# Kernel optimization log

Hardware: AMD Instinct MI355X
Metric: run time of the kernel (lower is better)

## Reference

```python
import jax, jax.numpy as jnp
import numpy as np

V_FEATS = 1024; N1 = 800; N2 = 800; K = 10
CONV = [256, 128]; DENSE = [256, 64]


def setup_inputs() -> dict:
    key = jax.random.key(0)
    ks = jax.random.split(key, 20)
    inp = {
        "Z1": jax.random.normal(ks[0], (N1, V_FEATS), jnp.float32),
        "nb1": jax.random.randint(ks[2], (N1, K), -1, N1),
        "Z2": jax.random.normal(ks[1], (N2, V_FEATS), jnp.float32),
        "nb2": jax.random.randint(ks[3], (N2, K), -1, N2),
    }
    j = 4
    dims = [V_FEATS] + CONV
    for i, (di, do) in enumerate(zip(dims[:-1], dims[1:])):
        s = 1.0 / np.sqrt(di)
        inp[f"Wr{i}"] = jax.random.normal(ks[j], (di, do), jnp.float32) * s; j += 1
        inp[f"Wnr{i}"] = jax.random.normal(ks[j], (di, do), jnp.float32) * s; j += 1
    fdims = [2 * CONV[-1]] + DENSE + [1]
    for i, (di, do) in enumerate(zip(fdims[:-1], fdims[1:])):
        s = 1.0 / np.sqrt(di)
        inp[f"fW{i}"] = jax.random.normal(ks[j], (di, do), jnp.float32) * s; j += 1
        inp[f"fb{i}"] = jnp.zeros((do,), jnp.float32)
    return inp


def gnn_layer(Z, nb, Wr, Wnr):
    # residue (self) signal and neighbor base signal
    res = Z @ Wr                                  # [N, F]
    base = Z @ Wnr                                # [N, F]
    mask = nb > -1                                # [N, K]
    feats = base[nb] * mask[..., None]            # gather (neg idx wrap, masked out)
    norm = jnp.maximum(mask.sum(1), 1).astype(Z.dtype)  # [N], avoid div-by-0
    return jax.nn.relu(res + feats.sum(1) / norm[:, None])


def _forward(Z1, nb1, Z2, nb2, Wr0, Wnr0, Wr1, Wnr1, fW0, fb0, fW1, fb1, fW2, fb2):
    # two stacked GNN layers per protein (shared weights across the two proteins)
    x1 = gnn_layer(gnn_layer(Z1, nb1, Wr0, Wnr0), nb1, Wr1, Wnr1)  # [N1, F]
    x2 = gnn_layer(gnn_layer(Z2, nb2, Wr0, Wnr0), nb2, Wr1, Wnr1)  # [N2, F]
    n1, F = x1.shape
    n2 = x2.shape[0]
    # all-pairs concat: itertools.product(rows(x1), rows(x2)) -> [N1*N2, 2F]
    pairs = jnp.concatenate(
        [jnp.broadcast_to(x1[:, None, :], (n1, n2, F)),
         jnp.broadcast_to(x2[None, :, :], (n1, n2, F))], axis=-1
    ).reshape(n1 * n2, 2 * F)
    h = jax.nn.relu(pairs @ fW0 + fb0)
    h = jax.nn.relu(h @ fW1 + fb1)
    return jnp.squeeze(h @ fW2 + fb2)             # [N1*N2]


def reference(Z1, nb1, Z2, nb2, Wr0, Wnr0, Wr1, Wnr1, fW0, fb0, fW1, fb1, fW2, fb2):
    return _forward(Z1, nb1, Z2, nb2, Wr0, Wnr0, Wr1, Wnr1,
                    fW0, fb0, fW1, fb1, fW2, fb2)
```

## Files before the change

### kernel.cpp

```cpp
#include <hip/hip_runtime.h>
#include <hip/hip_bf16.h>
#include <cstdint>
#include <cstddef>


typedef __bf16 bf16_t;
typedef __bf16 bf16x4 __attribute__((ext_vector_type(4)));
typedef __bf16 bf16x8 __attribute__((ext_vector_type(8)));
typedef float f32x4 __attribute__((ext_vector_type(4)));
typedef _Float16 f16_t;
typedef _Float16 f16x8 __attribute__((ext_vector_type(8)));

static __device__ __forceinline__ f32x4 mfma_bf16(bf16x8 a, bf16x8 b, f32x4 c) {
  return __builtin_amdgcn_mfma_f32_16x16x32_bf16(a, b, c, 0, 0, 0);
}
static __device__ __forceinline__ f32x4 mfma_f16(f16x8 a, f16x8 b, f32x4 c) {
  return __builtin_amdgcn_mfma_f32_16x16x32_f16(a, b, c, 0, 0, 0);
}

#define N1R 800
#define NR  1600
#define VF  1024
#define F0  256
#define F1  128

static __device__ __forceinline__ void split8(float4 va, float4 vb,
                                              bf16x8& h8, bf16x8& l8) {
  float v[8] = {va.x, va.y, va.z, va.w, vb.x, vb.y, vb.z, vb.w};
  #pragma unroll
  for (int e = 0; e < 8; ++e) {
    bf16_t h = (bf16_t)v[e];
    h8[e] = h;
    l8[e] = (bf16_t)(v[e] - (float)h);
  }
}

__global__ void conv_agg(const float* __restrict__ Z1, const float* __restrict__ Z2,
                         const int* __restrict__ nb1, const int* __restrict__ nb2,
                         const float* __restrict__ Wr0, const float* __restrict__ Wnr0,
                         const float* __restrict__ Wr1, const float* __restrict__ Wnr1,
                         const float* __restrict__ fW0, const float* __restrict__ fW1,
                         const float* __restrict__ fb1, const float* __restrict__ fW2,
                         const float* __restrict__ fb2,
                         bf16_t* __restrict__ W0h, bf16_t* __restrict__ W0l,
                         bf16_t* __restrict__ W1h, bf16_t* __restrict__ W1l,
                         bf16_t* __restrict__ fAh, bf16_t* __restrict__ fAl,
                         bf16_t* __restrict__ fBh, bf16_t* __restrict__ fBl,
                         f16_t* __restrict__ fW1th, float* __restrict__ fbw,
                         bf16_t* __restrict__ Zah, bf16_t* __restrict__ Zal) {
  int wb = blockIdx.x;
  int tid = threadIdx.x;
  if (wb >= 2625) {
    int r = wb - 2625;
    const int* nbp;
    const float* Zp;
    if (r < N1R) { nbp = nb1 + r * 10; Zp = Z1; }
    else         { nbp = nb2 + (r - N1R) * 10; Zp = Z2; }
    int c4 = tid * 4;
    float4 s = make_float4(0.f, 0.f, 0.f, 0.f);
    int cnt = 0;
    #pragma unroll
    for (int k = 0; k < 10; ++k) {
      int idx = nbp[k];
      if (idx > -1) {
        cnt++;
        float4 v = *(const float4*)(Zp + (size_t)idx * VF + c4);
        s.x += v.x; s.y += v.y; s.z += v.z; s.w += v.w;
      }
    }
    float inv = 1.f / (float)(cnt > 0 ? cnt : 1);
    float vv[4] = {s.x * inv, s.y * inv, s.z * inv, s.w * inv};
    bf16x4 h4, l4;
    #pragma unroll
    for (int e = 0; e < 4; ++e) {
      bf16_t h = (bf16_t)vv[e];
      h4[e] = h;
      l4[e] = (bf16_t)(vv[e] - (float)h);
    }
    *(bf16x4*)(Zah + (size_t)r * VF + c4) = h4;
    *(bf16x4*)(Zal + (size_t)r * VF + c4) = l4;
    return;
  }
  if (wb >= 2560 && wb < 2624) {
    int t = (wb - 2560) * 256 + tid;
    int n = t & 63;
    int k = t >> 6;
    fW1th[(n << 8) + k] = (f16_t)fW1[k * 64 + n];
    return;
  }
  if (wb == 2624) {
    if (tid < 128) {
      int jl = tid & 15, s = tid >> 4;
      fbw[jl * 8 + s] = (s < 4) ? fb1[s * 16 + jl] : fW2[(s - 4) * 16 + jl];
    } else if (tid == 128) {
      fbw[128] = fb2[0];
    }
    return;
  }
  const float* src; bf16_t* dh; bf16_t* dl; int ld, lk, ln, b0;
  if      (wb < 1024) { src = Wr0;  ld = 256; lk = 10; ln = 8; dh = W0h;              dl = W0l;              b0 = 0;    }
  else if (wb < 2048) { src = Wnr0; ld = 256; lk = 10; ln = 8; dh = W0h + 256 * 1024; dl = W0l + 256 * 1024; b0 = 1024; }
  else if (wb < 2176) { src = Wr1;  ld = 128; lk = 8;  ln = 7; dh = W1h;              dl = W1l;              b0 = 2048; }
  else if (wb < 2304) { src = Wnr1; ld = 128; lk = 8;  ln = 7; dh = W1h + 128 * 256;  dl = W1l + 128 * 256;  b0 = 2176; }
  else if (wb < 2432) { src = fW0;             ld = 256; lk = 7; ln = 8; dh = fAh;    dl = fAl;              b0 = 2304; }
  else                { src = fW0 + 128 * 256; ld = 256; lk = 7; ln = 8; dh = fBh;    dl = fBl;              b0 = 2432; }
  int t = (wb - b0) * 256 + tid;
  int n = t & ((1 << ln) - 1);
  int k = t >> ln;
  float v = src[k * ld + n];
  bf16_t h = (bf16_t)v;
  dh[(n << lk) + k] = h;
  dl[(n << lk) + k] = (bf16_t)(v - (float)h);
}

#define STEP6(ah, al, b0h, b0l, b1h, b1l)        \
  acc0 = mfma_bf16(ah, b0h, acc0);               \
  acc1 = mfma_bf16(ah, b1h, acc1);               \
  acc0 = mfma_bf16(al, b0h, acc0);               \
  acc1 = mfma_bf16(al, b1h, acc1);               \
  acc0 = mfma_bf16(ah, b0l, acc0);               \
  acc1 = mfma_bf16(ah, b1l, acc1);

__global__ __launch_bounds__(256) void gemm_l1(
    const float* __restrict__ Z1, const float* __restrict__ Z2,
    const bf16_t* __restrict__ Zah, const bf16_t* __restrict__ Zal,
    const bf16_t* __restrict__ W0h, const bf16_t* __restrict__ W0l,
    bf16_t* __restrict__ H0h, bf16_t* __restrict__ H0l) {
  int lane = threadIdx.x & 63;
  int w = threadIdx.x >> 6;
  int wr = w >> 1, wc = w & 1;
  int jl = lane & 15, hi = lane >> 4;

  int row0 = blockIdx.y * 32 + wr * 16;
  int col0 = blockIdx.x * 64 + wc * 32;
  int r = row0 + jl;
  int c0 = col0 + jl, c1 = col0 + 16 + jl;

  const float* pZ = ((r < N1R) ? Z1 + (size_t)r * VF
                               : Z2 + (size_t)(r - N1R) * VF) + hi * 8;
  const bf16_t* pAh = Zah + (size_t)r * VF + hi * 8;
  const bf16_t* pAl = Zal + (size_t)r * VF + hi * 8;
  const bf16_t* pB0h = W0h + (size_t)c0 * 1024 + hi * 8;
  const bf16_t* pB1h = W0h + (size_t)c1 * 1024 + hi * 8;
  const bf16_t* pB0l = W0l + (size_t)c0 * 1024 + hi * 8;
  const bf16_t* pB1l = W0l + (size_t)c1 * 1024 + hi * 8;
  const size_t OFF = (size_t)256 * 1024;

  f32x4 acc0 = {}, acc1 = {};
  for (int kb = 0; kb < 1024; kb += 32) {
    bf16x8 ah, al;
    split8(*(const float4*)(pZ + kb), *(const float4*)(pZ + kb + 4), ah, al);
    bf16x8 b0h = *(const bf16x8*)(pB0h + kb);
    bf16x8 b1h = *(const bf16x8*)(pB1h + kb);
    bf16x8 b0l = *(const bf16x8*)(pB0l + kb);
    bf16x8 b1l = *(const bf16x8*)(pB1l + kb);
    STEP6(ah, al, b0h, b0l, b1h, b1l)
  }
  for (int kb = 0; kb < 1024; kb += 32) {
    bf16x8 ah = *(const bf16x8*)(pAh + kb);
    bf16x8 al = *(const bf16x8*)(pAl + kb);
    bf16x8 b0h = *(const bf16x8*)(pB0h + OFF + kb);
    bf16x8 b1h = *(const bf16x8*)(pB1h + OFF + kb);
    bf16x8 b0l = *(const bf16x8*)(pB0l + OFF + kb);
    bf16x8 b1l = *(const bf16x8*)(pB1l + OFF + kb);
    STEP6(ah, al, b0h, b0l, b1h, b1l)
  }

  f32x4 accs[2] = {acc0, acc1};
  #pragma unroll
  for (int nn = 0; nn < 2; ++nn) {
    int col = col0 + nn * 16 + jl;
    #pragma unroll
    for (int reg = 0; reg < 4; ++reg) {
      int row = row0 + hi * 4 + reg;
      float v = fmaxf(accs[nn][reg], 0.f);
      bf16_t h = (bf16_t)v;
      H0h[(size_t)row * F0 + col] = h;
      H0l[(size_t)row * F0 + col] = (bf16_t)(v - (float)h);
    }
  }
}

__global__ void agg1_kernel(const bf16_t* __restrict__ H0h, const bf16_t* __restrict__ H0l,
                            const int* __restrict__ nb1, const int* __restrict__ nb2,
                            bf16_t* __restrict__ Gah, bf16_t* __restrict__ Gal) {
  int r = blockIdx.x;
  int c = threadIdx.x;
  const int* nbp;
  int roff;
  if (r < N1R) { nbp = nb1 + r * 10; roff = 0; }
  else         { nbp = nb2 + (r - N1R) * 10; roff = N1R; }
  float s = 0.f; int cnt = 0;
  #pragma unroll
  for (int k = 0; k < 10; ++k) {
    int idx = nbp[k];
    if (idx > -1) {
      cnt++;
      size_t o = (size_t)(roff + idx) * F0 + c;
      s += (float)H0h[o] + (float)H0l[o];
    }
  }
  float v = s / (float)(cnt > 0 ? cnt : 1);
  bf16_t h = (bf16_t)v;
  Gah[(size_t)r * F0 + c] = h;
  Gal[(size_t)r * F0 + c] = (bf16_t)(v - (float)h);
}

__global__ __launch_bounds__(256) void gemm_l2(
    const bf16_t* __restrict__ H0h, const bf16_t* __restrict__ H0l,
    const bf16_t* __restrict__ Gah, const bf16_t* __restrict__ Gal,
    const bf16_t* __restrict__ W1h, const bf16_t* __restrict__ W1l,
    bf16_t* __restrict__ H1h, bf16_t* __restrict__ H1l) {
  int lane = threadIdx.x & 63;
  int w = threadIdx.x >> 6;
  int wr = w >> 1, wc = w & 1;
  int jl = lane & 15, hi = lane >> 4;

  int row0 = blockIdx.y * 32 + wr * 16;
  int col0 = blockIdx.x * 64 + wc * 32;
  int r = row0 + jl;
  int c0 = col0 + jl, c1 = col0 + 16 + jl;

  const bf16_t* pAh = H0h + (size_t)r * F0 + hi * 8;
  const bf16_t* pAl = H0l + (size_t)r * F0 + hi * 8;
  const bf16_t* pGh = Gah + (size_t)r * F0 + hi * 8;
  const bf16_t* pGl = Gal + (size_t)r * F0 + hi * 8;
  const bf16_t* pB0h = W1h + (size_t)c0 * 256 + hi * 8;
  const bf16_t* pB1h = W1h + (size_t)c1 * 256 + hi * 8;
  const bf16_t* pB0l = W1l + (size_t)c0 * 256 + hi * 8;
  const bf16_t* pB1l = W1l + (size_t)c1 * 256 + hi * 8;
  const size_t OFF = (size_t)128 * 256;

  f32x4 acc0 = {}, acc1 = {};
  for (int kb = 0; kb < 256; kb += 32) {
    bf16x8 ah = *(const bf16x8*)(pAh + kb);
    bf16x8 al = *(const bf16x8*)(pAl + kb);
    bf16x8 b0h = *(const bf16x8*)(pB0h + kb);
    bf16x8 b1h = *(const bf16x8*)(pB1h + kb);
    bf16x8 b0l = *(const bf16x8*)(pB0l + kb);
    bf16x8 b1l = *(const bf16x8*)(pB1l + kb);
    STEP6(ah, al, b0h, b0l, b1h, b1l)
  }
  for (int kb = 0; kb < 256; kb += 32) {
    bf16x8 ah = *(const bf16x8*)(pGh + kb);
    bf16x8 al = *(const bf16x8*)(pGl + kb);
    bf16x8 b0h = *(const bf16x8*)(pB0h + OFF + kb);
    bf16x8 b1h = *(const bf16x8*)(pB1h + OFF + kb);
    bf16x8 b0l = *(const bf16x8*)(pB0l + OFF + kb);
    bf16x8 b1l = *(const bf16x8*)(pB1l + OFF + kb);
    STEP6(ah, al, b0h, b0l, b1h, b1l)
  }

  f32x4 accs[2] = {acc0, acc1};
  #pragma unroll
  for (int nn = 0; nn < 2; ++nn) {
    int col = col0 + nn * 16 + jl;
    #pragma unroll
    for (int reg = 0; reg < 4; ++reg) {
      int row = row0 + hi * 4 + reg;
      float v = fmaxf(accs[nn][reg], 0.f);
      bf16_t h = (bf16_t)v;
      H1h[(size_t)row * F1 + col] = h;
      H1l[(size_t)row * F1 + col] = (bf16_t)(v - (float)h);
    }
  }
}

static __device__ __forceinline__ void gemm_body(
    const bf16_t* __restrict__ Ah, const bf16_t* __restrict__ Al,
    const bf16_t* __restrict__ Bth, const bf16_t* __restrict__ Btl,
    const float* __restrict__ bias, f16_t* __restrict__ Ch,
    int M, int N, int K, int row0b, int col0b) {
  int lane = threadIdx.x & 63;
  int w = threadIdx.x >> 6;
  int wr = w >> 1, wc = w & 1;
  int jl = lane & 15, hi = lane >> 4;

  int row0 = row0b + wr * 32;
  int col0 = col0b + wc * 32;

  int r0 = min(row0 + jl, M - 1);
  int r1 = min(row0 + 16 + jl, M - 1);
  int c0 = col0 + jl;
  int c1 = col0 + 16 + jl;

  const bf16_t* pA0h = Ah + (size_t)r0 * K + hi * 8;
  const bf16_t* pA1h = Ah + (size_t)r1 * K + hi * 8;
  const bf16_t* pA0l = Al + (size_t)r0 * K + hi * 8;
  const bf16_t* pA1l = Al + (size_t)r1 * K + hi * 8;
  const bf16_t* pB0h = Bth + (size_t)c0 * K + hi * 8;
  const bf16_t* pB1h = Bth + (size_t)c1 * K + hi * 8;
  const bf16_t* pB0l = Btl + (size_t)c0 * K + hi * 8;
  const bf16_t* pB1l = Btl + (size_t)c1 * K + hi * 8;

  f32x4 acc[2][2] = {};
  for (int kb = 0; kb < K; kb += 32) {
    bf16x8 a0h = *(const bf16x8*)(pA0h + kb);
    bf16x8 a1h = *(const bf16x8*)(pA1h + kb);
    bf16x8 a0l = *(const bf16x8*)(pA0l + kb);
    bf16x8 a1l = *(const bf16x8*)(pA1l + kb);
    bf16x8 b0h = *(const bf16x8*)(pB0h + kb);
    bf16x8 b1h = *(const bf16x8*)(pB1h + kb);
    bf16x8 b0l = *(const bf16x8*)(pB0l + kb);
    bf16x8 b1l = *(const bf16x8*)(pB1l + kb);

    acc[0][0] = mfma_bf16(a0h, b0h, acc[0][0]);
    acc[0][1] = mfma_bf16(a0h, b1h, acc[0][1]);
    acc[1][0] = mfma_bf16(a1h, b0h, acc[1][0]);
    acc[1][1] = mfma_bf16(a1h, b1h, acc[1][1]);

    acc[0][0] = mfma_bf16(a0l, b0h, acc[0][0]);
    acc[0][1] = mfma_bf16(a0l, b1h, acc[0][1]);
    acc[1][0] = mfma_bf16(a1l, b0h, acc[1][0]);
    acc[1][1] = mfma_bf16(a1l, b1h, acc[1][1]);

    acc[0][0] = mfma_bf16(a0h, b0l, acc[0][0]);
    acc[0][1] = mfma_bf16(a0h, b1l, acc[0][1]);
    acc[1][0] = mfma_bf16(a1h, b0l, acc[1][0]);
    acc[1][1] = mfma_bf16(a1h, b1l, acc[1][1]);
  }

  #pragma unroll
  for (int m = 0; m < 2; ++m) {
    #pragma unroll
    for (int nn = 0; nn < 2; ++nn) {
      int col = col0 + nn * 16 + jl;
      float bv = bias ? bias[col] : 0.f;
      #pragma unroll
      for (int reg = 0; reg < 4; ++reg) {
        int row = row0 + m * 16 + hi * 4 + reg;
        if (row < M) Ch[(size_t)row * N + col] = (f16_t)(acc[m][nn][reg] + bv);
      }
    }
  }
}

__global__ __launch_bounds__(256) void gemm_dual(
    const bf16_t* __restrict__ H1h, const bf16_t* __restrict__ H1l,
    const bf16_t* __restrict__ fAh, const bf16_t* __restrict__ fAl,
    const bf16_t* __restrict__ fBh, const bf16_t* __restrict__ fBl,
    const float* __restrict__ fb0, f16_t* __restrict__ ABh) {
  int part = blockIdx.y / 13;
  int my = blockIdx.y % 13;
  gemm_body(H1h + (size_t)part * N1R * F1, H1l + (size_t)part * N1R * F1,
            part ? fBh : fAh, part ? fBl : fAl, part ? nullptr : fb0,
            ABh + (size_t)part * N1R * 256, N1R, 256, F1,
            my * 64, blockIdx.x * 64);
}

#define IBLK 2
#define ITILE 16
__global__ __launch_bounds__(256) void pair_kernel(
    const f16_t* __restrict__ ABh, const f16_t* __restrict__ W1th,
    const float* __restrict__ fbw, float* __restrict__ out) {
  __shared__ alignas(16) unsigned char sWh[64 * 512];
  __shared__ alignas(16) f16_t sA[ITILE * 256];

  const int tid = threadIdx.x;
  const int lane = tid & 63;
  const int w = tid >> 6;
  const int jl = lane & 15;
  const int hi = lane >> 4;
  const int j0 = blockIdx.x * 64;
  const int i0 = blockIdx.y * ITILE;

  #pragma unroll
  for (int s = 0; s < 8; ++s) {
    int c = tid + 256 * s;
    int n = c >> 5;
    int cb = (c & 31) << 4;
    int sw = cb ^ ((n & 7) << 4);
    *(uint4*)(sWh + n * 512 + sw) = *(const uint4*)((const unsigned char*)W1th + n * 512 + cb);
  }
  #pragma unroll
  for (int s = 0; s < 2; ++s) {
    int c = tid + 256 * s;
    int rr = c >> 5;
    int cc = c & 31;
    *(uint4*)((unsigned char*)sA + rr * 512 + cc * 16) =
        *(const uint4*)(ABh + (size_t)(i0 + rr) * 256 + cc * 8);
  }

  int j = j0 + w * 16 + jl;
  f16x8 breg[8];
  {
    const f16_t* Bp = ABh + (size_t)(N1R + j) * 256;
    bool ok = (j < N1R);
    f16x8 z{};
    #pragma unroll
    for (int t = 0; t < 8; ++t)
      breg[t] = ok ? *(const f16x8*)(Bp + t * 32 + hi * 8) : z;
  }

  float4 fb1r = *(const float4*)(fbw + jl * 8);
  float4 fw2r = *(const float4*)(fbw + jl * 8 + 4);
  float bias2 = fbw[128];

  __syncthreads();

  #pragma unroll 1
  for (int ig = 0; ig < ITILE / IBLK; ++ig) {
    f32x4 acc[IBLK][4] = {};
    #pragma unroll
    for (int t = 0; t < 8; ++t) {
      f16x8 bv = breg[t];
      f16x8 af[IBLK];
      const f16x8 Zv{};
      #pragma unroll
      for (int ib = 0; ib < IBLK; ++ib) {
        f16x8 av = *(const f16x8*)(sA + (ig * IBLK + ib) * 256 + t * 32 + hi * 8);
        af[ib] = __builtin_elementwise_max(av + bv, Zv);
      }
      int kbyte = t * 64 + hi * 16;
      #pragma unroll
      for (int nf = 0; nf < 4; ++nf) {
        int n = nf * 16 + jl;
        f16x8 wh = *(const f16x8*)(sWh + n * 512 + (kbyte ^ ((n & 7) << 4)));
        #pragma unroll
        for (int ib = 0; ib < IBLK; ++ib)
          acc[ib][nf] = mfma_f16(af[ib], wh, acc[ib][nf]);
      }
    }
    float fb1a[4] = {fb1r.x, fb1r.y, fb1r.z, fb1r.w};
    float fw2a[4] = {fw2r.x, fw2r.y, fw2r.z, fw2r.w};
    #pragma unroll
    for (int ib = 0; ib < IBLK; ++ib) {
      float part[4];
      #pragma unroll
      for (int r = 0; r < 4; ++r) {
        float ssum = 0.f;
        #pragma unroll
        for (int nf = 0; nf < 4; ++nf) {
          float h = acc[ib][nf][r] + fb1a[nf];
          h = fmaxf(h, 0.f);
          ssum += h * fw2a[nf];
        }
        part[r] = ssum;
      }
      #pragma unroll
      for (int off = 1; off < 16; off <<= 1) {
        #pragma unroll
        for (int r = 0; r < 4; ++r) part[r] += __shfl_xor(part[r], off, 64);
      }
      if (jl == 0) {
        int jo = j0 + w * 16 + hi * 4;
        if (jo < N1R) {
          float4 o = make_float4(part[0] + bias2, part[1] + bias2,
                                 part[2] + bias2, part[3] + bias2);
          *(float4*)(out + (size_t)(i0 + ig * IBLK + ib) * 800 + jo) = o;
        }
      }
    }
  }
}

extern "C" void kernel_launch(void* const* d_in, const int* in_sizes, int n_in,
                              void* d_out, int out_size, void* d_ws, size_t ws_size,
                              hipStream_t stream) {
  const float* Z1   = (const float*)d_in[0];
  const int*   nb1  = (const int*)d_in[1];
  const float* Z2   = (const float*)d_in[2];
  const int*   nb2  = (const int*)d_in[3];
  const float* Wr0  = (const float*)d_in[4];
  const float* Wnr0 = (const float*)d_in[5];
  const float* Wr1  = (const float*)d_in[6];
  const float* Wnr1 = (const float*)d_in[7];
  const float* fW0  = (const float*)d_in[8];
  const float* fb0  = (const float*)d_in[9];
  const float* fW1  = (const float*)d_in[10];
  const float* fb1  = (const float*)d_in[11];
  const float* fW2  = (const float*)d_in[12];
  const float* fb2  = (const float*)d_in[13];
  float* out = (float*)d_out;

  char* p = (char*)d_ws;
  auto alloc = [&](size_t bytes) {
    char* q = p;
    p += (bytes + 255) & ~(size_t)255;
    return q;
  };
  bf16_t* W0h   = (bf16_t*)alloc((size_t)512 * 1024 * 2);
  bf16_t* W0l   = (bf16_t*)alloc((size_t)512 * 1024 * 2);
  bf16_t* W1h   = (bf16_t*)alloc((size_t)256 * 256 * 2);
  bf16_t* W1l   = (bf16_t*)alloc((size_t)256 * 256 * 2);
  bf16_t* fAh   = (bf16_t*)alloc((size_t)256 * 128 * 2);
  bf16_t* fAl   = (bf16_t*)alloc((size_t)256 * 128 * 2);
  bf16_t* fBh   = (bf16_t*)alloc((size_t)256 * 128 * 2);
  bf16_t* fBl   = (bf16_t*)alloc((size_t)256 * 128 * 2);
  f16_t*  fW1th = (f16_t*)alloc((size_t)64 * 256 * 2);
  float*  fbw   = (float*)alloc(129 * 4);
  bf16_t* Zah   = (bf16_t*)alloc((size_t)NR * VF * 2);
  bf16_t* Zal   = (bf16_t*)alloc((size_t)NR * VF * 2);
  bf16_t* H0h   = (bf16_t*)alloc((size_t)NR * F0 * 2);
  bf16_t* H0l   = (bf16_t*)alloc((size_t)NR * F0 * 2);
  bf16_t* Gah   = (bf16_t*)alloc((size_t)NR * F0 * 2);
  bf16_t* Gal   = (bf16_t*)alloc((size_t)NR * F0 * 2);
  bf16_t* H1h   = (bf16_t*)alloc((size_t)NR * F1 * 2);
  bf16_t* H1l   = (bf16_t*)alloc((size_t)NR * F1 * 2);
  f16_t*  ABh   = (f16_t*)alloc((size_t)NR * 256 * 2);
  (void)in_sizes; (void)n_in; (void)out_size; (void)ws_size;

  conv_agg<<<4225, 256, 0, stream>>>(Z1, Z2, nb1, nb2, Wr0, Wnr0, Wr1, Wnr1,
                                     fW0, fW1, fb1, fW2, fb2,
                                     W0h, W0l, W1h, W1l, fAh, fAl, fBh, fBl,
                                     fW1th, fbw, Zah, Zal);
  gemm_l1<<<dim3(4, 50), 256, 0, stream>>>(Z1, Z2, Zah, Zal, W0h, W0l, H0h, H0l);
  agg1_kernel<<<NR, 256, 0, stream>>>(H0h, H0l, nb1, nb2, Gah, Gal);
  gemm_l2<<<dim3(2, 50), 256, 0, stream>>>(H0h, H0l, Gah, Gal, W1h, W1l, H1h, H1l);
  gemm_dual<<<dim3(4, 26), 256, 0, stream>>>(H1h, H1l, fAh, fAl, fBh, fBl, fb0, ABh);
  pair_kernel<<<dim3(13, 50), 256, 0, stream>>>(ABh, fW1th, fbw, out);
}
```

Before: 120.4 us.

## Split layer-1 GEMM over K into fp32 partials and shrink GEMM tiles

The first-layer GEMM is split along its two K halves, the raw Z part and the aggregated Z part, using a third grid dimension. Each half writes fp32 partial sums, and the aggregation kernel now adds them, applies ReLU and makes the bf16 hi/lo split. The l1, l2 and dual GEMMs all move to 16x64 tiles with one 16x16 MFMA tile per wave, which multiplies the block count. This is meant to fill the 256 CUs, which the old 100–200 block grids left idle. In exchange it adds fp32 partial-buffer traffic, makes the neighbor gather read two fp32 arrays, and gives up operand reuse per wave.

```diff
diff --git a/kernel.cpp b/kernel.cpp
--- a/kernel.cpp
+++ b/kernel.cpp
@@ -113,83 +113,76 @@
   dl[(n << lk) + k] = (bf16_t)(v - (float)h);
 }
 
-#define STEP6(ah, al, b0h, b0l, b1h, b1l)        \
-  acc0 = mfma_bf16(ah, b0h, acc0);               \
-  acc1 = mfma_bf16(ah, b1h, acc1);               \
-  acc0 = mfma_bf16(al, b0h, acc0);               \
-  acc1 = mfma_bf16(al, b1h, acc1);               \
-  acc0 = mfma_bf16(ah, b0l, acc0);               \
-  acc1 = mfma_bf16(ah, b1l, acc1);
-
 __global__ __launch_bounds__(256) void gemm_l1(
     const float* __restrict__ Z1, const float* __restrict__ Z2,
     const bf16_t* __restrict__ Zah, const bf16_t* __restrict__ Zal,
     const bf16_t* __restrict__ W0h, const bf16_t* __restrict__ W0l,
-    bf16_t* __restrict__ H0h, bf16_t* __restrict__ H0l) {
+    float* __restrict__ P) {
   int lane = threadIdx.x & 63;
   int w = threadIdx.x >> 6;
-  int wr = w >> 1, wc = w & 1;
   int jl = lane & 15, hi = lane >> 4;
 
-  int row0 = blockIdx.y * 32 + wr * 16;
-  int col0 = blockIdx.x * 64 + wc * 32;
+  int row0 = blockIdx.y * 16;
+  int col = blockIdx.x * 64 + w * 16 + jl;
+  int z = blockIdx.z;
   int r = row0 + jl;
-  int c0 = col0 + jl, c1 = col0 + 16 + jl;
-
-  const float* pZ = ((r < N1R) ? Z1 + (size_t)r * VF
-                               : Z2 + (size_t)(r - N1R) * VF) + hi * 8;
-  const bf16_t* pAh = Zah + (size_t)r * VF + hi * 8;
-  const bf16_t* pAl = Zal + (size_t)r * VF + hi * 8;
-  const bf16_t* pB0h = W0h + (size_t)c0 * 1024 + hi * 8;
-  const bf16_t* pB1h = W0h + (size_t)c1 * 1024 + hi * 8;
-  const bf16_t* pB0l = W0l + (size_t)c0 * 1024 + hi * 8;
-  const bf16_t* pB1l = W0l + (size_t)c1 * 1024 + hi * 8;
-  const size_t OFF = (size_t)256 * 1024;
-
-  f32x4 acc0 = {}, acc1 = {};
-  for (int kb = 0; kb < 1024; kb += 32) {
-    bf16x8 ah, al;
-    split8(*(const float4*)(pZ + kb), *(const float4*)(pZ + kb + 4), ah, al);
-    bf16x8 b0h = *(const bf16x8*)(pB0h + kb);
-    bf16x8 b1h = *(const bf16x8*)(pB1h + kb);
-    bf16x8 b0l = *(const bf16x8*)(pB0l + kb);
-    bf16x8 b1l = *(const bf16x8*)(pB1l + kb);
-    STEP6(ah, al, b0h, b0l, b1h, b1l)
-  }
-  for (int kb = 0; kb < 1024; kb += 32) {
-    bf16x8 ah = *(const bf16x8*)(pAh + kb);
-    bf16x8 al = *(const bf16x8*)(pAl + kb);
-    bf16x8 b0h = *(const bf16x8*)(pB0h + OFF + kb);
-    bf16x8 b1h = *(const bf16x8*)(pB1h + OFF + kb);
-    bf16x8 b0l = *(const bf16x8*)(pB0l + OFF + kb);
-    bf16x8 b1l = *(const bf16x8*)(pB1l + OFF + kb);
-    STEP6(ah, al, b0h, b0l, b1h, b1l)
-  }
-
-  f32x4 accs[2] = {acc0, acc1};
-  #pragma unroll
-  for (int nn = 0; nn < 2; ++nn) {
-    int col = col0 + nn * 16 + jl;
-    #pragma unroll
-    for (int reg = 0; reg < 4; ++reg) {
-      int row = row0 + hi * 4 + reg;
-      float v = fmaxf(accs[nn][reg], 0.f);
-      bf16_t h = (bf16_t)v;
-      H0h[(size_t)row * F0 + col] = h;
-      H0l[(size_t)row * F0 + col] = (bf16_t)(v - (float)h);
-    }
-  }
-}
-
-__global__ void agg1_kernel(const bf16_t* __restrict__ H0h, const bf16_t* __restrict__ H0l,
+
+  const size_t WOFF = (size_t)z * 256 * 1024;
+  const bf16_t* pBh = W0h + WOFF + (size_t)col * 1024 + hi * 8;
+  const bf16_t* pBl = W0l + WOFF + (size_t)col * 1024 + hi * 8;
+
+  f32x4 acc = {};
+  if (z == 0) {
+    const float* pZ = ((r < N1R) ? Z1 + (size_t)r * VF
+                                 : Z2 + (size_t)(r - N1R) * VF) + hi * 8;
+    #pragma unroll 4
+    for (int kb = 0; kb < 1024; kb += 32) {
+      bf16x8 ah, al;
+      split8(*(const float4*)(pZ + kb), *(const float4*)(pZ + kb + 4), ah, al);
+      bf16x8 bh = *(const bf16x8*)(pBh + kb);
+      bf16x8 bl = *(const bf16x8*)(pBl + kb);
+      acc = mfma_bf16(ah, bh, acc);
+      acc = mfma_bf16(al, bh, acc);
+      acc = mfma_bf16(ah, bl, acc);
+    }
+  } else {
+    const bf16_t* pAh = Zah + (size_t)r * VF + hi * 8;
+    const bf16_t* pAl = Zal + (size_t)r * VF + hi * 8;
+    #pragma unroll 4
+    for (int kb = 0; kb < 1024; kb += 32) {
+      bf16x8 ah = *(const bf16x8*)(pAh + kb);
+      bf16x8 al = *(const bf16x8*)(pAl + kb);
+      bf16x8 bh = *(const bf16x8*)(pBh + kb);
+      bf16x8 bl = *(const bf16x8*)(pBl + kb);
+      acc = mfma_bf16(ah, bh, acc);
+      acc = mfma_bf16(al, bh, acc);
+      acc = mfma_bf16(ah, bl, acc);
+    }
+  }
+  float* Pz = P + (size_t)z * NR * F0;
+  #pragma unroll
+  for (int reg = 0; reg < 4; ++reg) {
+    int row = row0 + hi * 4 + reg;
+    Pz[(size_t)row * F0 + col] = acc[reg];
+  }
+}
+
+__global__ void agg1_kernel(const float* __restrict__ P,
                             const int* __restrict__ nb1, const int* __restrict__ nb2,
+                            bf16_t* __restrict__ H0h, bf16_t* __restrict__ H0l,
                             bf16_t* __restrict__ Gah, bf16_t* __restrict__ Gal) {
   int r = blockIdx.x;
   int c = threadIdx.x;
+  const float* P1 = P + (size_t)NR * F0;
   const int* nbp;
   int roff;
   if (r < N1R) { nbp = nb1 + r * 10; roff = 0; }
   else         { nbp = nb2 + (r - N1R) * 10; roff = N1R; }
+  size_t so = (size_t)r * F0 + c;
+  float v = fmaxf(P[so] + P1[so], 0.f);
+  bf16_t h = (bf16_t)v;
+  H0h[so] = h;
+  H0l[so] = (bf16_t)(v - (float)h);
   float s = 0.f; int cnt = 0;
   #pragma unroll
   for (int k = 0; k < 10; ++k) {
@@ -197,13 +190,13 @@
     if (idx > -1) {
       cnt++;
       size_t o = (size_t)(roff + idx) * F0 + c;
-      s += (float)H0h[o] + (float)H0l[o];
-    }
-  }
-  float v = s / (float)(cnt > 0 ? cnt : 1);
-  bf16_t h = (bf16_t)v;
-  Gah[(size_t)r * F0 + c] = h;
-  Gal[(size_t)r * F0 + c] = (bf16_t)(v - (float)h);
+      s += fmaxf(P[o] + P1[o], 0.f);
+    }
+  }
+  float g = s / (float)(cnt > 0 ? cnt : 1);
+  bf16_t gh = (bf16_t)g;
+  Gah[so] = gh;
+  Gal[so] = (bf16_t)(g - (float)gh);
 }
 
 __global__ __launch_bounds__(256) void gemm_l2(
@@ -213,125 +206,49 @@
     bf16_t* __restrict__ H1h, bf16_t* __restrict__ H1l) {
   int lane = threadIdx.x & 63;
   int w = threadIdx.x >> 6;
-  int wr = w >> 1, wc = w & 1;
   int jl = lane & 15, hi = lane >> 4;
 
-  int row0 = blockIdx.y * 32 + wr * 16;
-  int col0 = blockIdx.x * 64 + wc * 32;
+  int row0 = blockIdx.y * 16;
+  int col = blockIdx.x * 64 + w * 16 + jl;
   int r = row0 + jl;
-  int c0 = col0 + jl, c1 = col0 + 16 + jl;
 
   const bf16_t* pAh = H0h + (size_t)r * F0 + hi * 8;
   const bf16_t* pAl = H0l + (size_t)r * F0 + hi * 8;
   const bf16_t* pGh = Gah + (size_t)r * F0 + hi * 8;
   const bf16_t* pGl = Gal + (size_t)r * F0 + hi * 8;
-  const bf16_t* pB0h = W1h + (size_t)c0 * 256 + hi * 8;
-  const bf16_t* pB1h = W1h + (size_t)c1 * 256 + hi * 8;
-  const bf16_t* pB0l = W1l + (size_t)c0 * 256 + hi * 8;
-  const bf16_t* pB1l = W1l + (size_t)c1 * 256 + hi * 8;
+  const bf16_t* pBh = W1h + (size_t)col * 256 + hi * 8;
+  const bf16_t* pBl = W1l + (size_t)col * 256 + hi * 8;
   const size_t OFF = (size_t)128 * 256;
 
-  f32x4 acc0 = {}, acc1 = {};
+  f32x4 acc = {};
+  #pragma unroll 2
   for (int kb = 0; kb < 256; kb += 32) {
     bf16x8 ah = *(const bf16x8*)(pAh + kb);
     bf16x8 al = *(const bf16x8*)(pAl + kb);
-    bf16x8 b0h = *(const bf16x8*)(pB0h + kb);
-    bf16x8 b1h = *(const bf16x8*)(pB1h + kb);
-    bf16x8 b0l = *(const bf16x8*)(pB0l + kb);
-    bf16x8 b1l = *(const bf16x8*)(pB1l + kb);
-    STEP6(ah, al, b0h, b0l, b1h, b1l)
-  }
+    bf16x8 bh = *(const bf16x8*)(pBh + kb);
+    bf16x8 bl = *(const bf16x8*)(pBl + kb);
+    acc = mfma_bf16(ah, bh, acc);
+    acc = mfma_bf16(al, bh, acc);
+    acc = mfma_bf16(ah, bl, acc);
+  }
+  #pragma unroll 2
   for (int kb = 0; kb < 256; kb += 32) {
     bf16x8 ah = *(const bf16x8*)(pGh + kb);
     bf16x8 al = *(const bf16x8*)(pGl + kb);
-    bf16x8 b0h = *(const bf16x8*)(pB0h + OFF + kb);
-    bf16x8 b1h = *(const bf16x8*)(pB1h + OFF + kb);
-    bf16x8 b0l = *(const bf16x8*)(pB0l + OFF + kb);
-    bf16x8 b1l = *(const bf16x8*)(pB1l + OFF + kb);
-    STEP6(ah, al, b0h, b0l, b1h, b1l)
-  }
-
-  f32x4 accs[2] = {acc0, acc1};
-  #pragma unroll
-  for (int nn = 0; nn < 2; ++nn) {
-    int col = col0 + nn * 16 + jl;
-    #pragma unroll
-    for (int reg = 0; reg < 4; ++reg) {
-      int row = row0 + hi * 4 + reg;
-      float v = fmaxf(accs[nn][reg], 0.f);
-      bf16_t h = (bf16_t)v;
-      H1h[(size_t)row * F1 + col] = h;
-      H1l[(size_t)row * F1 + col] = (bf16_t)(v - (float)h);
-    }
-  }
-}
-
-static __device__ __forceinline__ void gemm_body(
-    const bf16_t* __restrict__ Ah, const bf16_t* __restrict__ Al,
-    const bf16_t* __restrict__ Bth, const bf16_t* __restrict__ Btl,
-    const float* __restrict__ bias, f16_t* __restrict__ Ch,
-    int M, int N, int K, int row0b, int col0b) {
-  int lane = threadIdx.x & 63;
-  int w = threadIdx.x >> 6;
-  int wr = w >> 1, wc = w & 1;
-  int jl = lane & 15, hi = lane >> 4;
-
-  int row0 = row0b + wr * 32;
-  int col0 = col0b + wc * 32;
-
-  int r0 = min(row0 + jl, M - 1);
-  int r1 = min(row0 + 16 + jl, M - 1);
-  int c0 = col0 + jl;
-  int c1 = col0 + 16 + jl;
-
-  const bf16_t* pA0h = Ah + (size_t)r0 * K + hi * 8;
-  const bf16_t* pA1h = Ah + (size_t)r1 * K + hi * 8;
-  const bf16_t* pA0l = Al + (size_t)r0 * K + hi * 8;
-  const bf16_t* pA1l = Al + (size_t)r1 * K + hi * 8;
-  const bf16_t* pB0h = Bth + (size_t)c0 * K + hi * 8;
-  const bf16_t* pB1h = Bth + (size_t)c1 * K + hi * 8;
-  const bf16_t* pB0l = Btl + (size_t)c0 * K + hi * 8;
-  const bf16_t* pB1l = Btl + (size_t)c1 * K + hi * 8;
-
-  f32x4 acc[2][2] = {};
-  for (int kb = 0; kb < K; kb += 32) {
-    bf16x8 a0h = *(const bf16x8*)(pA0h + kb);
-    bf16x8 a1h = *(const bf16x8*)(pA1h + kb);
-    bf16x8 a0l = *(const bf16x8*)(pA0l + kb);
-    bf16x8 a1l = *(const bf16x8*)(pA1l + kb);
-    bf16x8 b0h = *(const bf16x8*)(pB0h + kb);
-    bf16x8 b1h = *(const bf16x8*)(pB1h + kb);
-    bf16x8 b0l = *(const bf16x8*)(pB0l + kb);
-    bf16x8 b1l = *(const bf16x8*)(pB1l + kb);
-
-    acc[0][0] = mfma_bf16(a0h, b0h, acc[0][0]);
-    acc[0][1] = mfma_bf16(a0h, b1h, acc[0][1]);
-    acc[1][0] = mfma_bf16(a1h, b0h, acc[1][0]);
-    acc[1][1] = mfma_bf16(a1h, b1h, acc[1][1]);
-
-    acc[0][0] = mfma_bf16(a0l, b0h, acc[0][0]);
-    acc[0][1] = mfma_bf16(a0l, b1h, acc[0][1]);
-    acc[1][0] = mfma_bf16(a1l, b0h, acc[1][0]);
-    acc[1][1] = mfma_bf16(a1l, b1h, acc[1][1]);
-
-    acc[0][0] = mfma_bf16(a0h, b0l, acc[0][0]);
-    acc[0][1] = mfma_bf16(a0h, b1l, acc[0][1]);
-    acc[1][0] = mfma_bf16(a1h, b0l, acc[1][0]);
-    acc[1][1] = mfma_bf16(a1h, b1l, acc[1][1]);
-  }
-
-  #pragma unroll
-  for (int m = 0; m < 2; ++m) {
-    #pragma unroll
-    for (int nn = 0; nn < 2; ++nn) {
-      int col = col0 + nn * 16 + jl;
-      float bv = bias ? bias[col] : 0.f;
-      #pragma unroll
-      for (int reg = 0; reg < 4; ++reg) {
-        int row = row0 + m * 16 + hi * 4 + reg;
-        if (row < M) Ch[(size_t)row * N + col] = (f16_t)(acc[m][nn][reg] + bv);
-      }
-    }
+    bf16x8 bh = *(const bf16x8*)(pBh + OFF + kb);
+    bf16x8 bl = *(const bf16x8*)(pBl + OFF + kb);
+    acc = mfma_bf16(ah, bh, acc);
+    acc = mfma_bf16(al, bh, acc);
+    acc = mfma_bf16(ah, bl, acc);
+  }
+
+  #pragma unroll
+  for (int reg = 0; reg < 4; ++reg) {
+    int row = row0 + hi * 4 + reg;
+    float v = fmaxf(acc[reg], 0.f);
+    bf16_t h = (bf16_t)v;
+    H1h[(size_t)row * F1 + col] = h;
+    H1l[(size_t)row * F1 + col] = (bf16_t)(v - (float)h);
   }
 }
 
@@ -340,12 +257,45 @@
     const bf16_t* __restrict__ fAh, const bf16_t* __restrict__ fAl,
     const bf16_t* __restrict__ fBh, const bf16_t* __restrict__ fBl,
     const float* __restrict__ fb0, f16_t* __restrict__ ABh) {
-  int part = blockIdx.y / 13;
-  int my = blockIdx.y % 13;
-  gemm_body(H1h + (size_t)part * N1R * F1, H1l + (size_t)part * N1R * F1,
-            part ? fBh : fAh, part ? fBl : fAl, part ? nullptr : fb0,
-            ABh + (size_t)part * N1R * 256, N1R, 256, F1,
-            my * 64, blockIdx.x * 64);
+  int lane = threadIdx.x & 63;
+  int w = threadIdx.x >> 6;
+  int jl = lane & 15, hi = lane >> 4;
+
+  int part = blockIdx.y / 50;
+  int my = blockIdx.y % 50;
+  int row0 = my * 16;
+  int col = blockIdx.x * 64 + w * 16 + jl;
+  int r = row0 + jl;
+
+  const bf16_t* Ah = H1h + (size_t)part * N1R * F1;
+  const bf16_t* Al = H1l + (size_t)part * N1R * F1;
+  const bf16_t* Bh = part ? fBh : fAh;
+  const bf16_t* Bl = part ? fBl : fAl;
+
+  const bf16_t* pAh = Ah + (size_t)r * F1 + hi * 8;
+  const bf16_t* pAl = Al + (size_t)r * F1 + hi * 8;
+  const bf16_t* pBh = Bh + (size_t)col * F1 + hi * 8;
+  const bf16_t* pBl = Bl + (size_t)col * F1 + hi * 8;
+
+  f32x4 acc = {};
+  #pragma unroll
+  for (int kb = 0; kb < 128; kb += 32) {
+    bf16x8 ah = *(const bf16x8*)(pAh + kb);
+    bf16x8 al = *(const bf16x8*)(pAl + kb);
+    bf16x8 bh = *(const bf16x8*)(pBh + kb);
+    bf16x8 bl = *(const bf16x8*)(pBl + kb);
+    acc = mfma_bf16(ah, bh, acc);
+    acc = mfma_bf16(al, bh, acc);
+    acc = mfma_bf16(ah, bl, acc);
+  }
+
+  float bv = part ? 0.f : fb0[col];
+  f16_t* C = ABh + (size_t)part * N1R * 256;
+  #pragma unroll
+  for (int reg = 0; reg < 4; ++reg) {
+    int row = row0 + hi * 4 + reg;
+    C[(size_t)row * 256 + col] = (f16_t)(acc[reg] + bv);
+  }
 }
 
 #define IBLK 2
@@ -491,6 +441,7 @@
   float*  fbw   = (float*)alloc(129 * 4);
   bf16_t* Zah   = (bf16_t*)alloc((size_t)NR * VF * 2);
   bf16_t* Zal   = (bf16_t*)alloc((size_t)NR * VF * 2);
+  float*  P01   = (float*)alloc((size_t)2 * NR * F0 * 4);
   bf16_t* H0h   = (bf16_t*)alloc((size_t)NR * F0 * 2);
   bf16_t* H0l   = (bf16_t*)alloc((size_t)NR * F0 * 2);
   bf16_t* Gah   = (bf16_t*)alloc((size_t)NR * F0 * 2);
@@ -504,9 +455,9 @@
                                      fW0, fW1, fb1, fW2, fb2,
                                      W0h, W0l, W1h, W1l, fAh, fAl, fBh, fBl,
                                      fW1th, fbw, Zah, Zal);
-  gemm_l1<<<dim3(4, 50), 256, 0, stream>>>(Z1, Z2, Zah, Zal, W0h, W0l, H0h, H0l);
-  agg1_kernel<<<NR, 256, 0, stream>>>(H0h, H0l, nb1, nb2, Gah, Gal);
-  gemm_l2<<<dim3(2, 50), 256, 0, stream>>>(H0h, H0l, Gah, Gal, W1h, W1l, H1h, H1l);
-  gemm_dual<<<dim3(4, 26), 256, 0, stream>>>(H1h, H1l, fAh, fAl, fBh, fBl, fb0, ABh);
+  gemm_l1<<<dim3(4, 100, 2), 256, 0, stream>>>(Z1, Z2, Zah, Zal, W0h, W0l, P01);
+  agg1_kernel<<<NR, 256, 0, stream>>>(P01, nb1, nb2, H0h, H0l, Gah, Gal);
+  gemm_l2<<<dim3(2, 100), 256, 0, stream>>>(H0h, H0l, Gah, Gal, W1h, W1l, H1h, H1l);
+  gemm_dual<<<dim3(4, 100), 256, 0, stream>>>(H1h, H1l, fAh, fAl, fBh, fBl, fb0, ABh);
   pair_kernel<<<dim3(13, 50), 256, 0, stream>>>(ABh, fW1th, fbw, out);
 }
```

Result: slower. 130.1 us (+8.1%).
